# Kernel optimization log

Measured on AMD Instinct MI355X. Metric: run time of the kernel, lower is better.

Reference implementation:

```python
import jax, jax.numpy as jnp
import numpy as np

B, S, E = 4, 4096, 1024
H = 16
D = E // H            # per-head dim (k_dim == v_dim == 64)
N_SAMPLE = 1024       # tokens kept per (batch, head)


def setup_inputs() -> dict:
    key = jax.random.key(0)
    ks = jax.random.split(key, 7)
    lim = float(np.sqrt(6.0 / (E + E)))  # xavier_uniform for square weight
    x = jax.random.normal(ks[0], (B, S, E), dtype=jnp.float32)
    Wq = jax.random.uniform(ks[1], (E, E), jnp.float32, -lim, lim)
    Wk = jax.random.uniform(ks[2], (E, E), jnp.float32, -lim, lim)
    Wv = jax.random.uniform(ks[3], (E, E), jnp.float32, -lim, lim)
    bq = jnp.zeros((E,), jnp.float32)
    bk = jnp.zeros((E,), jnp.float32)
    bv = jnp.zeros((E,), jnp.float32)
    return {"x": x, "Wq": Wq, "bq": bq, "Wk": Wk, "bk": bk, "Wv": Wv, "bv": bv}


def reference(x, Wq, bq, Wk, bk, Wv, bv):
    Bs, Sl, Ed = x.shape
    # projections -> [B, H, S, D]
    q = (x @ Wq.T + bq).reshape(Bs, Sl, H, D).transpose(0, 2, 1, 3)
    k = (x @ Wk.T + bk).reshape(Bs, Sl, H, D).transpose(0, 2, 1, 3)
    v = (x @ Wv.T + bv).reshape(Bs, Sl, H, D).transpose(0, 2, 1, 3)

    # cosFormer feature map: relu + cos/sin positional reweighting
    pos = jnp.arange(Sl, dtype=x.dtype)
    theta = (jnp.pi / 2.0) * pos / Sl            # [S]
    cos_w = jnp.cos(theta)[None, None, :, None]  # [1,1,S,1]
    sin_w = jnp.sin(theta)[None, None, :, None]
    qn = jax.nn.relu(q)
    kn = jax.nn.relu(k)
    q_cos, q_sin = qn * cos_w, qn * sin_w
    k_cos, k_sin = kn * cos_w, kn * sin_w

    # token sampler: top-N_SAMPLE tokens by (q*k).sum(-1) per (b,h)
    scores = jnp.sum(q * k, axis=-1)             # [B,H,S]
    _, idx = jax.lax.top_k(scores, N_SAMPLE)     # [B,H,n]

    # global K^T V reductions: [B,H,D,D]
    kv_cos = jnp.einsum("bhsd,bhse->bhde", k_cos, v)
    kv_sin = jnp.einsum("bhsd,bhse->bhde", k_sin, v)

    # gather sampled queries: [B,H,n,D]
    qs_cos = jnp.take_along_axis(q_cos, idx[..., None], axis=2)
    qs_sin = jnp.take_along_axis(q_sin, idx[..., None], axis=2)

    sampled = (jnp.einsum("bhnd,bhde->bhne", qs_cos, kv_cos)
               + jnp.einsum("bhnd,bhde->bhne", qs_sin, kv_sin))  # [B,H,n,D]

    # scatter-add back into zeros at sampled positions
    bi = jnp.arange(Bs)[:, None, None]
    hi = jnp.arange(H)[None, :, None]
    values = jnp.zeros((Bs, H, Sl, D), sampled.dtype).at[bi, hi, idx].add(sampled)

    out = values.transpose(0, 2, 1, 3).reshape(Bs, Sl, H * D)
    return out  # o_proj is Identity (v_dim*num_heads == embed_dim); dropout=0
```

## Files before the change

kernel.cpp:

```cpp
#include <hip/hip_runtime.h>
#include <hip/hip_bf16.h>

#define B_ 4
#define S_ 4096
#define E_ 1024
#define H_ 16
#define D_ 64
#define NS_ 1024
#define M_ (B_*S_)
#define K_ E_
#define DELTA 0.12f
#define BANDCAP 96

typedef __attribute__((ext_vector_type(8))) short bf16x8;
typedef __attribute__((ext_vector_type(4))) float floatx4;
typedef __attribute__((ext_vector_type(2))) float f32x2;

#define THSTEP 0.00038349519697141023f

__device__ inline float bf16_to_f(unsigned short u) {
    return __uint_as_float(((unsigned)u) << 16);
}
__device__ inline unsigned short f_to_bf16(float f) {
    unsigned u = __float_as_uint(f);
    unsigned r = (u + 0x7FFFu + ((u >> 16) & 1u)) >> 16;
    return (unsigned short)r;
}

__device__ inline void gl_lds16(const void* g, void* l) {
    __builtin_amdgcn_global_load_lds(
        (const __attribute__((address_space(1))) void*)g,
        (__attribute__((address_space(3))) void*)l, 16, 0, 0);
}

__global__ __launch_bounds__(256) void split_x_kernel(
    const float* __restrict__ x, ushort* __restrict__ xh)
{
    int i = blockIdx.x * 256 + threadIdx.x;
    float4 v = ((const float4*)x)[i];
    ushort4 hh;
    hh.x = f_to_bf16(v.x); hh.y = f_to_bf16(v.y);
    hh.z = f_to_bf16(v.z); hh.w = f_to_bf16(v.w);
    ((ushort4*)xh)[i] = hh;
}

__global__ __launch_bounds__(256) void split_w_kernel(
    const float* __restrict__ Wq, const float* __restrict__ Wk,
    const float* __restrict__ Wv,
    ushort* __restrict__ Wqh, ushort* __restrict__ Wql,
    ushort* __restrict__ Wkh, ushort* __restrict__ Wkl,
    ushort* __restrict__ Wvh)
{
    int i = blockIdx.x * 256 + threadIdx.x;
    float4 q = ((const float4*)Wq)[i];
    float4 k = ((const float4*)Wk)[i];
    float4 v = ((const float4*)Wv)[i];
    ushort4 h, l;
    h.x=f_to_bf16(q.x); l.x=f_to_bf16(q.x-bf16_to_f(h.x));
    h.y=f_to_bf16(q.y); l.y=f_to_bf16(q.y-bf16_to_f(h.y));
    h.z=f_to_bf16(q.z); l.z=f_to_bf16(q.z-bf16_to_f(h.z));
    h.w=f_to_bf16(q.w); l.w=f_to_bf16(q.w-bf16_to_f(h.w));
    ((ushort4*)Wqh)[i]=h; ((ushort4*)Wql)[i]=l;
    h.x=f_to_bf16(k.x); l.x=f_to_bf16(k.x-bf16_to_f(h.x));
    h.y=f_to_bf16(k.y); l.y=f_to_bf16(k.y-bf16_to_f(h.y));
    h.z=f_to_bf16(k.z); l.z=f_to_bf16(k.z-bf16_to_f(h.z));
    h.w=f_to_bf16(k.w); l.w=f_to_bf16(k.w-bf16_to_f(h.w));
    ((ushort4*)Wkh)[i]=h; ((ushort4*)Wkl)[i]=l;
    h.x=f_to_bf16(v.x); h.y=f_to_bf16(v.y);
    h.z=f_to_bf16(v.z); h.w=f_to_bf16(v.w);
    ((ushort4*)Wvh)[i]=h;
}

__global__ __launch_bounds__(256) void qkv_gemm(
    const ushort* __restrict__ xh,
    const ushort* __restrict__ Wqh, const ushort* __restrict__ Wql,
    const ushort* __restrict__ Wkh, const ushort* __restrict__ Wkl,
    const ushort* __restrict__ Wvh,
    const float* __restrict__ bq, const float* __restrict__ bk,
    const float* __restrict__ bv,
    float* __restrict__ q32, float* __restrict__ k32, ushort* __restrict__ v16)
{
    __shared__ __align__(16) ushort As[128 * 64];
    __shared__ __align__(16) ushort Bsh[128 * 64];
    __shared__ __align__(16) ushort Bsl[128 * 64];

    const int w = blockIdx.z;
    const ushort* Bhp = (w == 0) ? Wqh : (w == 1) ? Wkh : Wvh;
    const ushort* Blp = (w == 0) ? Wql : Wkl;
    const float* bias = (w == 0) ? bq : (w == 1) ? bk : bv;
    const bool lo = (w < 2);

    const int m0 = blockIdx.x * 128;
    const int n0 = blockIdx.y * 128;
    const int t = threadIdx.x;
    const int wave = t >> 6, lane = t & 63;
    const int wm = (wave >> 1) * 64, wn = (wave & 1) * 64;
    const int m16 = lane & 15, quad = lane >> 4;

    floatx4 acc[4][4];
#pragma unroll
    for (int i = 0; i < 4; i++)
#pragma unroll
        for (int j = 0; j < 4; j++) acc[i][j] = (floatx4){0.f, 0.f, 0.f, 0.f};

    int aoff[4], boff[4], lbase[4];
#pragma unroll
    for (int i = 0; i < 4; i++) {
        int slot = i * 256 + t;
        int r = slot >> 3, c = slot & 7, g = c ^ (r & 7);
        aoff[i] = (m0 + r) * K_ + g * 8;
        boff[i] = (n0 + r) * K_ + g * 8;
        lbase[i] = (i * 256 + wave * 64) * 8;
    }

    for (int ks = 0; ks < 16; ++ks) {
        const int kcol = ks * 64;
#pragma unroll
        for (int i = 0; i < 4; i++) {
            gl_lds16(xh + aoff[i] + kcol, &As[lbase[i]]);
            gl_lds16(Bhp + boff[i] + kcol, &Bsh[lbase[i]]);
        }
        if (lo) {
#pragma unroll
            for (int i = 0; i < 4; i++)
                gl_lds16(Blp + boff[i] + kcol, &Bsl[lbase[i]]);
        }
        __syncthreads();

#pragma unroll
        for (int kk = 0; kk < 2; ++kk) {
            bf16x8 af[4], bfr[4];
            const int g = kk * 4 + quad;
#pragma unroll
            for (int mt = 0; mt < 4; ++mt) {
                int r = wm + mt * 16 + m16;
                af[mt] = *(const bf16x8*)&As[(r * 8 + (g ^ (r & 7))) * 8];
            }
#pragma unroll
            for (int nt = 0; nt < 4; ++nt) {
                int r2 = wn + nt * 16 + m16;
                bfr[nt] = *(const bf16x8*)&Bsh[(r2 * 8 + (g ^ (r2 & 7))) * 8];
            }
#pragma unroll
            for (int mt = 0; mt < 4; ++mt)
#pragma unroll
                for (int nt = 0; nt < 4; ++nt)
                    acc[mt][nt] = __builtin_amdgcn_mfma_f32_16x16x32_bf16(
                        af[mt], bfr[nt], acc[mt][nt], 0, 0, 0);
            if (lo) {
#pragma unroll
                for (int nt = 0; nt < 4; ++nt) {
                    int r2 = wn + nt * 16 + m16;
                    bfr[nt] = *(const bf16x8*)&Bsl[(r2 * 8 + (g ^ (r2 & 7))) * 8];
                }
#pragma unroll
                for (int mt = 0; mt < 4; ++mt)
#pragma unroll
                    for (int nt = 0; nt < 4; ++nt)
                        acc[mt][nt] = __builtin_amdgcn_mfma_f32_16x16x32_bf16(
                            af[mt], bfr[nt], acc[mt][nt], 0, 0, 0);
            }
        }
        __syncthreads();
    }

    float biasv[4];
#pragma unroll
    for (int nt = 0; nt < 4; nt++)
        biasv[nt] = bias[n0 + wn + nt * 16 + m16];

    if (w < 2) {
        float* dst = (w == 0) ? q32 : k32;
#pragma unroll
        for (int mt = 0; mt < 4; ++mt)
#pragma unroll
            for (int nt = 0; nt < 4; ++nt) {
                int colg = n0 + wn + nt * 16 + m16;
#pragma unroll
                for (int reg = 0; reg < 4; ++reg) {
                    int rowg = m0 + wm + mt * 16 + quad * 4 + reg;
                    dst[(size_t)rowg * E_ + colg] = acc[mt][nt][reg] + biasv[nt];
                }
            }
    } else {
#pragma unroll
        for (int mt = 0; mt < 4; ++mt)
#pragma unroll
            for (int nt = 0; nt < 4; ++nt) {
                int colg = n0 + wn + nt * 16 + m16;
#pragma unroll
                for (int reg = 0; reg < 4; ++reg) {
                    int rowg = m0 + wm + mt * 16 + quad * 4 + reg;
                    v16[(size_t)rowg * E_ + colg] = f_to_bf16(acc[mt][nt][reg] + biasv[nt]);
                }
            }
    }
}

__global__ __launch_bounds__(256) void scores_kernel(
    const float* __restrict__ q32, const float* __restrict__ k32,
    float* __restrict__ scores)
{
    int g = blockIdx.x * 16 + (threadIdx.x >> 4);
    int sub = threadIdx.x & 15;
    int s = g & (S_ - 1);
    int bh = g >> 12;
    int b = bh >> 4, h = bh & 15;
    size_t addr = (size_t)(b * S_ + s) * E_ + h * 64 + sub * 4;
    float4 qv = *(const float4*)(q32 + addr);
    float4 kv = *(const float4*)(k32 + addr);
    float p = qv.x * kv.x + qv.y * kv.y + qv.z * kv.z + qv.w * kv.w;
#pragma unroll
    for (int m = 8; m; m >>= 1) p += __shfl_xor(p, m, 64);
    if (sub == 0) scores[g] = p;
}

__global__ __launch_bounds__(256) void band_select_kernel(
    const float* __restrict__ scores, int* __restrict__ selidx,
    int* __restrict__ band, int* __restrict__ meta)
{
    __shared__ unsigned keys[4096];
    __shared__ unsigned hist[256];
    __shared__ unsigned suf[256];
    __shared__ unsigned bcast[2];
    __shared__ int cnt_in, cnt_band;

    int bh = blockIdx.x;
    int t = threadIdx.x;
    const float* sc = scores + (size_t)bh * S_;

    for (int i = t; i < 4096; i += 256) {
        unsigned u = __float_as_uint(sc[i]);
        u = (u & 0x80000000u) ? ~u : (u | 0x80000000u);
        keys[i] = u;
    }
    if (t == 0) { cnt_in = 0; cnt_band = 0; }
    __syncthreads();

    unsigned prefix = 0, want = NS_;
    for (int shift = 24; shift >= 0; shift -= 8) {
        hist[t] = 0;
        __syncthreads();
        unsigned pmask = (shift == 24) ? 0u : (0xFFFFFFFFu << (shift + 8));
        for (int i = t; i < 4096; i += 256) {
            unsigned ky = keys[i];
            if ((ky & pmask) == prefix) atomicAdd(&hist[(ky >> shift) & 255u], 1u);
        }
        __syncthreads();
        suf[t] = hist[t];
        __syncthreads();
        for (int off = 1; off < 256; off <<= 1) {
            unsigned add = (t + off < 256) ? suf[t + off] : 0u;
            __syncthreads();
            suf[t] += add;
            __syncthreads();
        }
        unsigned Sb = suf[t];
        unsigned Snx = (t < 255) ? suf[t + 1] : 0u;
        if (Sb >= want && Snx < want) {
            bcast[0] = (unsigned)t;
            bcast[1] = want - Snx;
        }
        __syncthreads();
        prefix = prefix | (bcast[0] << shift);
        want = bcast[1];
        __syncthreads();
    }
    unsigned fb = (prefix & 0x80000000u) ? (prefix ^ 0x80000000u) : ~prefix;
    float Ta = __uint_as_float(fb);
    float Thi = Ta + DELTA, Tlo = Ta - DELTA;

    int* sel = selidx + (size_t)bh * NS_;
    int* bnd = band + (size_t)bh * BANDCAP;
    for (int i = t; i < 4096; i += 256) {
        float v = sc[i];
        if (v > Thi) {
            int p = atomicAdd(&cnt_in, 1);
            sel[p] = i;
        } else if (v >= Tlo) {
            int p = atomicAdd(&cnt_band, 1);
            if (p < BANDCAP) bnd[p] = i;
        }
    }
    __syncthreads();
    if (t == 0) {
        meta[bh * 2 + 0] = cnt_in;
        meta[bh * 2 + 1] = (cnt_band < BANDCAP) ? cnt_band : BANDCAP;
    }
}

__global__ __launch_bounds__(512) void band_exact_kernel(
    const float* __restrict__ x,
    const float* __restrict__ Wq, const float* __restrict__ Wk,
    const int* __restrict__ band, const int* __restrict__ meta,
    double* __restrict__ bscore)
{
    int j = blockIdx.x, bh = blockIdx.y;
    int NB = meta[bh * 2 + 1];
    if (j >= NB) return;
    int b = bh >> 4, h = bh & 15;
    int s = band[(size_t)bh * BANDCAP + j];
    int t = threadIdx.x;
    int wave = t >> 6, lane = t & 63;

    __shared__ float xs[1024];
    __shared__ double qkd[128];

    if (t < 256)
        *(float4*)&xs[t * 4] = *(const float4*)(x + (size_t)(b * S_ + s) * K_ + t * 4);
    __syncthreads();

    const float* Wbase = (wave < 4) ? Wq : Wk;
    int role = wave >> 2;
    int dbase = (wave & 3) * 16;
    const float4* xs4 = (const float4*)xs;

    for (int rr = 0; rr < 16; ++rr) {
        int d = dbase + rr;
        const float4* wrow4 = (const float4*)(Wbase + (size_t)(h * 64 + d) * K_);
        double a0 = 0.0, a1 = 0.0, a2 = 0.0, a3 = 0.0;
#pragma unroll
        for (int p = 0; p < 4; ++p) {
            float4 wv = wrow4[lane + 64 * p];
            float4 xv = xs4[lane + 64 * p];
            a0 += (double)xv.x * wv.x;
            a1 += (double)xv.y * wv.y;
            a2 += (double)xv.z * wv.z;
            a3 += (double)xv.w * wv.w;
        }
        double a = (a0 + a1) + (a2 + a3);
#pragma unroll
        for (int m = 32; m; m >>= 1) a += __shfl_xor(a, m, 64);
        if (lane == 0) qkd[role * 64 + d] = a;
    }
    __syncthreads();

    if (t < 64) {
        double p = qkd[t] * qkd[64 + t];
#pragma unroll
        for (int m = 32; m; m >>= 1) p += __shfl_xor(p, m, 64);
        if (t == 0) bscore[(size_t)bh * BANDCAP + j] = p;
    }
}

__global__ __launch_bounds__(128) void band_rank_kernel(
    const double* __restrict__ bscore, const int* __restrict__ band,
    const int* __restrict__ meta, int* __restrict__ selidx)
{
    __shared__ double sc[BANDCAP];
    __shared__ int bi[BANDCAP];
    int bh = blockIdx.x, t = threadIdx.x;
    int cnt_in = meta[bh * 2 + 0], NB = meta[bh * 2 + 1];
    int need = NS_ - cnt_in;
    if (t < NB) {
        sc[t] = bscore[(size_t)bh * BANDCAP + t];
        bi[t] = band[(size_t)bh * BANDCAP + t];
    }
    __syncthreads();
    if (t < NB) {
        double mine = sc[t]; int myi = bi[t]; int r = 0;
        for (int j2 = 0; j2 < NB; ++j2)
            r += (sc[j2] > mine) || (sc[j2] == mine && bi[j2] < myi);
        if (r < need) selidx[(size_t)bh * NS_ + cnt_in + r] = myi;
    }
}

__global__ __launch_bounds__(256) void kv_partial_kernel(
    const float* __restrict__ k32, const ushort* __restrict__ v16,
    float* __restrict__ kvp)
{
    __shared__ float kls[16 * 64];
    __shared__ float vls[16 * 64];
    int ch = blockIdx.x;
    int bh = blockIdx.y;
    int b = bh >> 4, h = bh & 15;
    int t = threadIdx.x;
    int d0 = (t >> 4) * 4, e0 = (t & 15) * 4;
    int lr = t >> 4, lc = (t & 15) * 4;

    f32x2 accC[4][2] = {}, accS[4][2] = {};
    const float* kbase = k32 + (size_t)b * S_ * E_ + h * 64;
    const ushort* vbase = v16 + (size_t)b * S_ * E_ + h * 64;
    int s0 = ch * 256;

    for (int g = 0; g < 16; ++g) {
        int srow = s0 + g * 16 + lr;
        float4 kf = *(const float4*)(kbase + (size_t)srow * E_ + lc);
        ushort4 vu = *(const ushort4*)(vbase + (size_t)srow * E_ + lc);
        __syncthreads();
        *(float4*)&kls[lr * 64 + lc] = kf;
        float4 vf = { bf16_to_f(vu.x), bf16_to_f(vu.y),
                      bf16_to_f(vu.z), bf16_to_f(vu.w) };
        *(float4*)&vls[lr * 64 + lc] = vf;
        __syncthreads();
#pragma unroll 4
        for (int si = 0; si < 16; ++si) {
            int s = s0 + g * 16 + si;
            float th = (float)s * THSTEP;
            float cw = __cosf(th), sw = __sinf(th);
            float4 kf2 = *(const float4*)&kls[si * 64 + d0];
            float4 vf2 = *(const float4*)&vls[si * 64 + e0];
            float kr[4] = { fmaxf(kf2.x, 0.f), fmaxf(kf2.y, 0.f),
                            fmaxf(kf2.z, 0.f), fmaxf(kf2.w, 0.f) };
            f32x2 v01 = { vf2.x, vf2.y }, v23 = { vf2.z, vf2.w };
#pragma unroll
            for (int i = 0; i < 4; i++) {
                f32x2 kc2 = { kr[i] * cw, kr[i] * cw };
                f32x2 ks2 = { kr[i] * sw, kr[i] * sw };
                accC[i][0] += kc2 * v01;  accC[i][1] += kc2 * v23;
                accS[i][0] += ks2 * v01;  accS[i][1] += ks2 * v23;
            }
        }
    }
    float* pc = kvp + ((size_t)(bh * 16 + ch) * 2) * 4096;
    float* ps = pc + 4096;
#pragma unroll
    for (int i = 0; i < 4; i++) {
        pc[(d0 + i) * 64 + e0 + 0] = accC[i][0][0];
        pc[(d0 + i) * 64 + e0 + 1] = accC[i][0][1];
        pc[(d0 + i) * 64 + e0 + 2] = accC[i][1][0];
        pc[(d0 + i) * 64 + e0 + 3] = accC[i][1][1];
        ps[(d0 + i) * 64 + e0 + 0] = accS[i][0][0];
        ps[(d0 + i) * 64 + e0 + 1] = accS[i][0][1];
        ps[(d0 + i) * 64 + e0 + 2] = accS[i][1][0];
        ps[(d0 + i) * 64 + e0 + 3] = accS[i][1][1];
    }
}

__global__ __launch_bounds__(256) void kv_reduce_kernel(
    const float* __restrict__ kvp, float* __restrict__ kv)
{
    int i = blockIdx.x * 256 + threadIdx.x;
    if (i >= 64 * 2 * 4096) return;
    int bh = i >> 13;
    int rem = i & 8191;
    const float* p = kvp + (size_t)bh * 16 * 8192 + rem;
    float a = 0.f;
#pragma unroll
    for (int c = 0; c < 16; c++) a += p[c * 8192];
    kv[i] = a;
}

__global__ __launch_bounds__(256) void sampled_kernel(
    const float* __restrict__ q32, const int* __restrict__ selidx,
    const float* __restrict__ kv, float* __restrict__ out)
{
    __shared__ __align__(16) float kvc[4096];
    __shared__ __align__(16) float kvs[4096];
    __shared__ __align__(16) float qs[64 * 68];
    __shared__ int sidx[64];
    int bh = blockIdx.y;
    int b = bh >> 4, h = bh & 15;
    int t = threadIdx.x;

    const float4* kvsrc4 = (const float4*)(kv + (size_t)bh * 8192);
    float4* kvc4 = (float4*)kvc;
    float4* kvs4 = (float4*)kvs;
#pragma unroll
    for (int i = 0; i < 4; ++i) {
        kvc4[i * 256 + t] = kvsrc4[i * 256 + t];
        kvs4[i * 256 + t] = kvsrc4[1024 + i * 256 + t];
    }
    if (t < 64) sidx[t] = selidx[(size_t)bh * NS_ + blockIdx.x * 64 + t];
    __syncthreads();

#pragma unroll
    for (int c = 0; c < 4; ++c) {
        int i = c * 256 + t;
        int row = i >> 4, qp = i & 15;
        int sr = sidx[row];
        *(float4*)&qs[row * 68 + qp * 4] =
            *(const float4*)(q32 + (size_t)(b * S_ + sr) * E_ + h * 64 + qp * 4);
    }
    __syncthreads();

    int tok = t >> 2, eq = t & 3;
    int sr = sidx[tok];
    float th = (float)sr * THSTEP;
    float cw = __cosf(th), sw = __sinf(th);

    f32x2 acc2[8];
#pragma unroll
    for (int e = 0; e < 8; e++) acc2[e] = (f32x2){0.f, 0.f};

    const float4* kvcb = (const float4*)&kvc[eq * 16];
    const float4* kvsb = (const float4*)&kvs[eq * 16];
    for (int d = 0; d < 64; ++d) {
        float qd = fmaxf(qs[tok * 68 + d], 0.f);
        f32x2 a2 = { qd * cw, qd * cw };
        f32x2 b2 = { qd * sw, qd * sw };
#pragma unroll
        for (int c = 0; c < 4; ++c) {
            float4 c4 = kvcb[d * 16 + c];
            float4 s4 = kvsb[d * 16 + c];
            f32x2 c01 = { c4.x, c4.y }, c23 = { c4.z, c4.w };
            f32x2 s01 = { s4.x, s4.y }, s23 = { s4.z, s4.w };
            acc2[c * 2 + 0] += a2 * c01 + b2 * s01;
            acc2[c * 2 + 1] += a2 * c23 + b2 * s23;
        }
    }

    float* dst = out + (size_t)(b * S_ + sr) * E_ + h * 64 + eq * 16;
#pragma unroll
    for (int c = 0; c < 4; ++c) {
        float4 o = { acc2[c * 2 + 0][0], acc2[c * 2 + 0][1],
                     acc2[c * 2 + 1][0], acc2[c * 2 + 1][1] };
        *(float4*)(dst + c * 4) = o;
    }
}

__global__ void zero_kernel(uint4* __restrict__ p, int n16)
{
    int stride = gridDim.x * blockDim.x;
    for (int i = blockIdx.x * blockDim.x + threadIdx.x; i < n16; i += stride)
        p[i] = make_uint4(0u, 0u, 0u, 0u);
}

extern "C" void kernel_launch(void* const* d_in, const int* in_sizes, int n_in,
                              void* d_out, int out_size, void* d_ws, size_t ws_size,
                              hipStream_t stream)
{
    const float* x  = (const float*)d_in[0];
    const float* Wq = (const float*)d_in[1];
    const float* bq = (const float*)d_in[2];
    const float* Wk = (const float*)d_in[3];
    const float* bk = (const float*)d_in[4];
    const float* Wv = (const float*)d_in[5];
    const float* bv = (const float*)d_in[6];

    char* ws = (char*)d_ws;
    ushort* xh     = (ushort*)(ws);
    float*  kvp    = (float*)(ws);
    float*  q32    = (float*)(ws + 33554432);
    float*  k32    = (float*)(ws + 100663296);
    ushort* v16    = (ushort*)(ws + 167772160);
    ushort* Wqh    = (ushort*)(ws + 201326592);
    ushort* Wql    = (ushort*)(ws + 203423744);
    ushort* Wkh    = (ushort*)(ws + 205520896);
    ushort* Wkl    = (ushort*)(ws + 207618048);
    ushort* Wvh    = (ushort*)(ws + 209715200);
    float*  scores = (float*)(ws + 211812352);
    int*    selidx = (int*)(ws + 212860928);
    int*    band   = (int*)(ws + 213123072);
    double* bscore = (double*)(ws + 213147648);
    int*    meta   = (int*)(ws + 213196800);
    float*  kv     = (float*)(ws + 213197312);
    float*  out    = (float*)d_out;

    hipLaunchKernelGGL(zero_kernel, dim3(2048), dim3(256), 0, stream,
                       (uint4*)out, (int)((size_t)M_ * E_ * 4 / 16));
    hipLaunchKernelGGL(split_x_kernel, dim3((M_ * K_) / 1024), dim3(256), 0, stream,
                       x, xh);
    hipLaunchKernelGGL(split_w_kernel, dim3((E_ * E_) / 1024), dim3(256), 0, stream,
                       Wq, Wk, Wv, Wqh, Wql, Wkh, Wkl, Wvh);
    hipLaunchKernelGGL(qkv_gemm, dim3(128, 8, 3), dim3(256), 0, stream,
                       xh, Wqh, Wql, Wkh, Wkl, Wvh, bq, bk, bv, q32, k32, v16);
    hipLaunchKernelGGL(scores_kernel, dim3((B_ * H_ * S_) / 16), dim3(256), 0, stream,
                       q32, k32, scores);
    hipLaunchKernelGGL(band_select_kernel, dim3(B_ * H_), dim3(256), 0, stream,
                       scores, selidx, band, meta);
    hipLaunchKernelGGL(band_exact_kernel, dim3(BANDCAP, B_ * H_), dim3(512), 0, stream,
                       x, Wq, Wk, band, meta, bscore);
    hipLaunchKernelGGL(band_rank_kernel, dim3(B_ * H_), dim3(128), 0, stream,
                       bscore, band, meta, selidx);
    hipLaunchKernelGGL(kv_partial_kernel, dim3(16, 64), dim3(256), 0, stream,
                       k32, v16, kvp);
    hipLaunchKernelGGL(kv_reduce_kernel, dim3(2048), dim3(256), 0, stream,
                       kvp, kv);
    hipLaunchKernelGGL(sampled_kernel, dim3(NS_ / 64, B_ * H_), dim3(256), 0, stream,
                       q32, selidx, kv, out);
}
```

Baseline: 562.4 us.

## Fuse prep kernels, template QKV GEMM by precision, rewrite kv accumulators as scalars

Merges the output zeroing, x bf16 conversion and weight hi/lo split into one prep kernel, removing two launches. Splits the combined QKV GEMM into three launches of a templated kernel. The V variant drops the low-part LDS buffer and its branches, which lowers its LDS footprint and can raise occupancy. The kv_partial accumulators move from packed float2 vectors to scalar floats, which may change how the compiler schedules the FMAs. Separate GEMM launches give up concurrency between the Q, K and V blocks and add launch overhead.

```diff
diff --git a/kernel.cpp b/kernel.cpp
--- a/kernel.cpp
+++ b/kernel.cpp
@@ -33,62 +33,62 @@
         (__attribute__((address_space(3))) void*)l, 16, 0, 0);
 }
 
-__global__ __launch_bounds__(256) void split_x_kernel(
-    const float* __restrict__ x, ushort* __restrict__ xh)
-{
-    int i = blockIdx.x * 256 + threadIdx.x;
-    float4 v = ((const float4*)x)[i];
-    ushort4 hh;
-    hh.x = f_to_bf16(v.x); hh.y = f_to_bf16(v.y);
-    hh.z = f_to_bf16(v.z); hh.w = f_to_bf16(v.w);
-    ((ushort4*)xh)[i] = hh;
-}
-
-__global__ __launch_bounds__(256) void split_w_kernel(
+__global__ __launch_bounds__(256) void prep_kernel(
+    const float* __restrict__ x,
     const float* __restrict__ Wq, const float* __restrict__ Wk,
     const float* __restrict__ Wv,
+    ushort* __restrict__ xh,
     ushort* __restrict__ Wqh, ushort* __restrict__ Wql,
     ushort* __restrict__ Wkh, ushort* __restrict__ Wkl,
-    ushort* __restrict__ Wvh)
-{
-    int i = blockIdx.x * 256 + threadIdx.x;
-    float4 q = ((const float4*)Wq)[i];
-    float4 k = ((const float4*)Wk)[i];
-    float4 v = ((const float4*)Wv)[i];
-    ushort4 h, l;
-    h.x=f_to_bf16(q.x); l.x=f_to_bf16(q.x-bf16_to_f(h.x));
-    h.y=f_to_bf16(q.y); l.y=f_to_bf16(q.y-bf16_to_f(h.y));
-    h.z=f_to_bf16(q.z); l.z=f_to_bf16(q.z-bf16_to_f(h.z));
-    h.w=f_to_bf16(q.w); l.w=f_to_bf16(q.w-bf16_to_f(h.w));
-    ((ushort4*)Wqh)[i]=h; ((ushort4*)Wql)[i]=l;
-    h.x=f_to_bf16(k.x); l.x=f_to_bf16(k.x-bf16_to_f(h.x));
-    h.y=f_to_bf16(k.y); l.y=f_to_bf16(k.y-bf16_to_f(h.y));
-    h.z=f_to_bf16(k.z); l.z=f_to_bf16(k.z-bf16_to_f(h.z));
-    h.w=f_to_bf16(k.w); l.w=f_to_bf16(k.w-bf16_to_f(h.w));
-    ((ushort4*)Wkh)[i]=h; ((ushort4*)Wkl)[i]=l;
-    h.x=f_to_bf16(v.x); h.y=f_to_bf16(v.y);
-    h.z=f_to_bf16(v.z); h.w=f_to_bf16(v.w);
-    ((ushort4*)Wvh)[i]=h;
-}
-
-__global__ __launch_bounds__(256) void qkv_gemm(
+    ushort* __restrict__ Wvh,
+    uint4* __restrict__ outz)
+{
+    int t = blockIdx.x * 256 + threadIdx.x;
+    uint4 z = make_uint4(0u, 0u, 0u, 0u);
+#pragma unroll
+    for (int c = 0; c < 4; ++c)
+        outz[c * 1048576 + t] = z;
+#pragma unroll
+    for (int c = 0; c < 4; ++c) {
+        int i = c * 1048576 + t;
+        float4 v = ((const float4*)x)[i];
+        ushort4 hh;
+        hh.x = f_to_bf16(v.x); hh.y = f_to_bf16(v.y);
+        hh.z = f_to_bf16(v.z); hh.w = f_to_bf16(v.w);
+        ((ushort4*)xh)[i] = hh;
+    }
+    if (t < 262144) {
+        int i = t;
+        float4 q = ((const float4*)Wq)[i];
+        float4 k = ((const float4*)Wk)[i];
+        float4 v = ((const float4*)Wv)[i];
+        ushort4 h, l;
+        h.x=f_to_bf16(q.x); l.x=f_to_bf16(q.x-bf16_to_f(h.x));
+        h.y=f_to_bf16(q.y); l.y=f_to_bf16(q.y-bf16_to_f(h.y));
+        h.z=f_to_bf16(q.z); l.z=f_to_bf16(q.z-bf16_to_f(h.z));
+        h.w=f_to_bf16(q.w); l.w=f_to_bf16(q.w-bf16_to_f(h.w));
+        ((ushort4*)Wqh)[i]=h; ((ushort4*)Wql)[i]=l;
+        h.x=f_to_bf16(k.x); l.x=f_to_bf16(k.x-bf16_to_f(h.x));
+        h.y=f_to_bf16(k.y); l.y=f_to_bf16(k.y-bf16_to_f(h.y));
+        h.z=f_to_bf16(k.z); l.z=f_to_bf16(k.z-bf16_to_f(h.z));
+        h.w=f_to_bf16(k.w); l.w=f_to_bf16(k.w-bf16_to_f(h.w));
+        ((ushort4*)Wkh)[i]=h; ((ushort4*)Wkl)[i]=l;
+        h.x=f_to_bf16(v.x); h.y=f_to_bf16(v.y);
+        h.z=f_to_bf16(v.z); h.w=f_to_bf16(v.w);
+        ((ushort4*)Wvh)[i]=h;
+    }
+}
+
+template<int LO>
+__global__ __launch_bounds__(256) void qkv_gemm_t(
     const ushort* __restrict__ xh,
-    const ushort* __restrict__ Wqh, const ushort* __restrict__ Wql,
-    const ushort* __restrict__ Wkh, const ushort* __restrict__ Wkl,
-    const ushort* __restrict__ Wvh,
-    const float* __restrict__ bq, const float* __restrict__ bk,
-    const float* __restrict__ bv,
-    float* __restrict__ q32, float* __restrict__ k32, ushort* __restrict__ v16)
+    const ushort* __restrict__ Bhp, const ushort* __restrict__ Blp,
+    const float* __restrict__ bias,
+    float* __restrict__ o32, ushort* __restrict__ o16)
 {
     __shared__ __align__(16) ushort As[128 * 64];
     __shared__ __align__(16) ushort Bsh[128 * 64];
-    __shared__ __align__(16) ushort Bsl[128 * 64];
-
-    const int w = blockIdx.z;
-    const ushort* Bhp = (w == 0) ? Wqh : (w == 1) ? Wkh : Wvh;
-    const ushort* Blp = (w == 0) ? Wql : Wkl;
-    const float* bias = (w == 0) ? bq : (w == 1) ? bk : bv;
-    const bool lo = (w < 2);
+    __shared__ __align__(16) ushort Bsl[LO ? 128 * 64 : 8];
 
     const int m0 = blockIdx.x * 128;
     const int n0 = blockIdx.y * 128;
@@ -120,7 +120,7 @@
             gl_lds16(xh + aoff[i] + kcol, &As[lbase[i]]);
             gl_lds16(Bhp + boff[i] + kcol, &Bsh[lbase[i]]);
         }
-        if (lo) {
+        if constexpr (LO) {
 #pragma unroll
             for (int i = 0; i < 4; i++)
                 gl_lds16(Blp + boff[i] + kcol, &Bsl[lbase[i]]);
@@ -147,7 +147,7 @@
                 for (int nt = 0; nt < 4; ++nt)
                     acc[mt][nt] = __builtin_amdgcn_mfma_f32_16x16x32_bf16(
                         af[mt], bfr[nt], acc[mt][nt], 0, 0, 0);
-            if (lo) {
+            if constexpr (LO) {
 #pragma unroll
                 for (int nt = 0; nt < 4; ++nt) {
                     int r2 = wn + nt * 16 + m16;
@@ -169,8 +169,7 @@
     for (int nt = 0; nt < 4; nt++)
         biasv[nt] = bias[n0 + wn + nt * 16 + m16];
 
-    if (w < 2) {
-        float* dst = (w == 0) ? q32 : k32;
+    if constexpr (LO) {
 #pragma unroll
         for (int mt = 0; mt < 4; ++mt)
 #pragma unroll
@@ -179,7 +178,7 @@
 #pragma unroll
                 for (int reg = 0; reg < 4; ++reg) {
                     int rowg = m0 + wm + mt * 16 + quad * 4 + reg;
-                    dst[(size_t)rowg * E_ + colg] = acc[mt][nt][reg] + biasv[nt];
+                    o32[(size_t)rowg * E_ + colg] = acc[mt][nt][reg] + biasv[nt];
                 }
             }
     } else {
@@ -191,7 +190,7 @@
 #pragma unroll
                 for (int reg = 0; reg < 4; ++reg) {
                     int rowg = m0 + wm + mt * 16 + quad * 4 + reg;
-                    v16[(size_t)rowg * E_ + colg] = f_to_bf16(acc[mt][nt][reg] + biasv[nt]);
+                    o16[(size_t)rowg * E_ + colg] = f_to_bf16(acc[mt][nt][reg] + biasv[nt]);
                 }
             }
     }
@@ -378,7 +377,7 @@
     int d0 = (t >> 4) * 4, e0 = (t & 15) * 4;
     int lr = t >> 4, lc = (t & 15) * 4;
 
-    f32x2 accC[4][2] = {}, accS[4][2] = {};
+    float accC[4][4] = {}, accS[4][4] = {};
     const float* kbase = k32 + (size_t)b * S_ * E_ + h * 64;
     const ushort* vbase = v16 + (size_t)b * S_ * E_ + h * 64;
     int s0 = ch * 256;
@@ -402,29 +401,28 @@
             float4 vf2 = *(const float4*)&vls[si * 64 + e0];
             float kr[4] = { fmaxf(kf2.x, 0.f), fmaxf(kf2.y, 0.f),
                             fmaxf(kf2.z, 0.f), fmaxf(kf2.w, 0.f) };
-            f32x2 v01 = { vf2.x, vf2.y }, v23 = { vf2.z, vf2.w };
-#pragma unroll
-            for (int i = 0; i < 4; i++) {
-                f32x2 kc2 = { kr[i] * cw, kr[i] * cw };
-                f32x2 ks2 = { kr[i] * sw, kr[i] * sw };
-                accC[i][0] += kc2 * v01;  accC[i][1] += kc2 * v23;
-                accS[i][0] += ks2 * v01;  accS[i][1] += ks2 * v23;
-            }
+            float vv[4] = { vf2.x, vf2.y, vf2.z, vf2.w };
+            float kc[4], ksn[4];
+#pragma unroll
+            for (int i = 0; i < 4; i++) { kc[i] = kr[i] * cw; ksn[i] = kr[i] * sw; }
+#pragma unroll
+            for (int i = 0; i < 4; i++)
+#pragma unroll
+                for (int jj = 0; jj < 4; jj++) {
+                    accC[i][jj] += kc[i] * vv[jj];
+                    accS[i][jj] += ksn[i] * vv[jj];
+                }
         }
     }
     float* pc = kvp + ((size_t)(bh * 16 + ch) * 2) * 4096;
     float* ps = pc + 4096;
 #pragma unroll
-    for (int i = 0; i < 4; i++) {
-        pc[(d0 + i) * 64 + e0 + 0] = accC[i][0][0];
-        pc[(d0 + i) * 64 + e0 + 1] = accC[i][0][1];
-        pc[(d0 + i) * 64 + e0 + 2] = accC[i][1][0];
-        pc[(d0 + i) * 64 + e0 + 3] = accC[i][1][1];
-        ps[(d0 + i) * 64 + e0 + 0] = accS[i][0][0];
-        ps[(d0 + i) * 64 + e0 + 1] = accS[i][0][1];
-        ps[(d0 + i) * 64 + e0 + 2] = accS[i][1][0];
-        ps[(d0 + i) * 64 + e0 + 3] = accS[i][1][1];
-    }
+    for (int i = 0; i < 4; i++)
+#pragma unroll
+        for (int jj = 0; jj < 4; jj++) {
+            pc[(d0 + i) * 64 + (e0 + jj)] = accC[i][jj];
+            ps[(d0 + i) * 64 + (e0 + jj)] = accS[i][jj];
+        }
 }
 
 __global__ __launch_bounds__(256) void kv_reduce_kernel(
@@ -507,13 +505,6 @@
                      acc2[c * 2 + 1][0], acc2[c * 2 + 1][1] };
         *(float4*)(dst + c * 4) = o;
     }
-}
-
-__global__ void zero_kernel(uint4* __restrict__ p, int n16)
-{
-    int stride = gridDim.x * blockDim.x;
-    for (int i = blockIdx.x * blockDim.x + threadIdx.x; i < n16; i += stride)
-        p[i] = make_uint4(0u, 0u, 0u, 0u);
 }
 
 extern "C" void kernel_launch(void* const* d_in, const int* in_sizes, int n_in,
@@ -547,14 +538,14 @@
     float*  kv     = (float*)(ws + 213197312);
     float*  out    = (float*)d_out;
 
-    hipLaunchKernelGGL(zero_kernel, dim3(2048), dim3(256), 0, stream,
-                       (uint4*)out, (int)((size_t)M_ * E_ * 4 / 16));
-    hipLaunchKernelGGL(split_x_kernel, dim3((M_ * K_) / 1024), dim3(256), 0, stream,
-                       x, xh);
-    hipLaunchKernelGGL(split_w_kernel, dim3((E_ * E_) / 1024), dim3(256), 0, stream,
-                       Wq, Wk, Wv, Wqh, Wql, Wkh, Wkl, Wvh);
-    hipLaunchKernelGGL(qkv_gemm, dim3(128, 8, 3), dim3(256), 0, stream,
-                       xh, Wqh, Wql, Wkh, Wkl, Wvh, bq, bk, bv, q32, k32, v16);
+    hipLaunchKernelGGL(prep_kernel, dim3(4096), dim3(256), 0, stream,
+                       x, Wq, Wk, Wv, xh, Wqh, Wql, Wkh, Wkl, Wvh, (uint4*)out);
+    hipLaunchKernelGGL((qkv_gemm_t<1>), dim3(128, 8), dim3(256), 0, stream,
+                       xh, Wqh, Wql, bq, q32, (ushort*)nullptr);
+    hipLaunchKernelGGL((qkv_gemm_t<1>), dim3(128, 8), dim3(256), 0, stream,
+                       xh, Wkh, Wkl, bk, k32, (ushort*)nullptr);
+    hipLaunchKernelGGL((qkv_gemm_t<0>), dim3(128, 8), dim3(256), 0, stream,
+                       xh, Wvh, Wvh, bv, (float*)nullptr, v16);
     hipLaunchKernelGGL(scores_kernel, dim3((B_ * H_ * S_) / 16), dim3(256), 0, stream,
                        q32, k32, scores);
     hipLaunchKernelGGL(band_select_kernel, dim3(B_ * H_), dim3(256), 0, stream,
```

Measured after the change: 580.0 us. 1.03x slower.
